# Kernel optimization log

Hardware: AMD Instinct MI355X
Metric: run time of the kernel (lower is better)

The kernel has to match this reference:

```python
import jax, jax.numpy as jnp
import numpy as np

TAU = 1.0      # gumbel-softmax temperature
ALPHA = 0.05   # mixprop alpha
GDEP = 1       # mixprop depth

B, C, H, W = 16, 512, 96, 96
N = 64  # n_classes / codebook size


def setup_inputs() -> dict:
    key = jax.random.key(0)
    ks = jax.random.split(key, 8)
    u = jax.random.uniform(ks[3], (B, N, H, W), dtype=jnp.float32, minval=1e-6, maxval=1.0 - 1e-6)
    gumbel_noise = -jnp.log(-jnp.log(u))  # standard Gumbel(0,1)
    return {
        "x": jax.random.normal(ks[0], (B, C, H, W), dtype=jnp.float32),
        "centers": jax.random.normal(ks[1], (N, C), dtype=jnp.float32) * 0.1,
        "A": jax.random.uniform(ks[2], (N, N), dtype=jnp.float32),
        "gumbel_noise": gumbel_noise,
        "W_bc": jax.random.normal(ks[4], (1, C), dtype=jnp.float32) * 0.05,
        "b_bc": jnp.zeros((1,), dtype=jnp.float32),
        "W_gcn": jax.random.normal(ks[5], (C, 2 * C), dtype=jnp.float32) * 0.03,
        "b_gcn": jnp.zeros((C,), dtype=jnp.float32),
    }


def _mixprop_centers(centers, A, W_gcn, b_gcn):
    # mixprop on the codebook: centers [N, C] viewed as x of shape [1, C, N, 1]
    n = A.shape[0]
    adj = A + jnp.eye(n, dtype=A.dtype)
    a = adj / adj.sum(axis=1, keepdims=True)           # row-normalized adjacency
    xg = centers.T[None, :, :, None]                    # [1, C, N, 1]
    h = xg
    outs = [h]
    for _ in range(GDEP):
        h = ALPHA * xg + (1.0 - ALPHA) * jnp.einsum('ncwl,vw->ncvl', h, a)
        outs.append(h)
    ho = jnp.concatenate(outs, axis=1)                  # [1, (GDEP+1)*C, N, 1]
    new_c = jnp.einsum('oc,bcvl->bovl', W_gcn, ho) + b_gcn[None, :, None, None]
    return new_c[0, :, :, 0].T                          # [N, C]


def reference(x, centers, A, gumbel_noise, W_bc, b_bc, W_gcn, b_gcn):
    n = centers.shape[0]
    # inner products of features with codebook centers
    inner_products = jnp.einsum('bchw,nc->bnhw', x, centers)          # [B, N, H, W]
    # gumbel-softmax with hard (straight-through) assignment over dim 1
    y = jax.nn.softmax((inner_products + gumbel_noise) / TAU, axis=1)
    hard = jax.nn.one_hot(jnp.argmax(y, axis=1), n, dtype=y.dtype, axis=1)
    one_hot = hard + y - jax.lax.stop_gradient(y)
    # quantized features via codebook gather
    z_q = jnp.einsum('bnhw,nd->bdhw', one_hot, centers)               # [B, C, H, W]
    # 1x1 conv binary classifier + global average pool
    heatmap = jnp.einsum('oc,bchw->bohw', W_bc, z_q) + b_bc[None, :, None, None]  # [B,1,H,W]
    logits = heatmap.mean(axis=(2, 3)).squeeze()                      # [B]
    # graph diffusion of the codebook
    new_centers = _mixprop_centers(centers, A, W_gcn, b_gcn)          # [N, C]
    normed_ip = jnp.einsum('bchw,nc->bnhw', x, new_centers)           # [B, N, H, W]
    cluster_probs = jax.nn.one_hot(jnp.argmax(normed_ip, axis=1), n, dtype=normed_ip.dtype, axis=1)
    cluster_loss = -(cluster_probs * jax.nn.softmax(normed_ip, axis=1)).sum(axis=1).mean()
    return heatmap, logits, cluster_loss, inner_products
```

## Files before the change

### kernel.cpp

```cpp
#include <hip/hip_runtime.h>
#include <math.h>

#define BATCH   16
#define CDIM    512
#define HWDIM   9216
#define NCLS    64
#define TILE    128
#define NTILES  72
#define NCHUNK  16

#define LOGOFF  147456
#define LOSSOFF 147472
#define IPOFF   147473

#define WS_CC   0
#define WS_S    65536
#define WS_PH   65600
#define WS_PC   66752
#define WS_AP   67904
#define WS_MIX  166208

typedef __attribute__((ext_vector_type(8))) short bf16x8;
typedef __attribute__((ext_vector_type(4))) float f32x4;

__device__ __forceinline__ void split3(float v, float& h, float& m, float& l) {
  float hf = __uint_as_float(__float_as_uint(v) & 0xFFFF0000u);
  float r  = v - hf;
  float mf = __uint_as_float(__float_as_uint(r) & 0xFFFF0000u);
  float r2 = r - mf;
  float lf = __uint_as_float(__float_as_uint(r2) & 0xFFFF0000u);
  h = hf; m = mf; l = lf;
}

__device__ __forceinline__ unsigned packbf(float a, float b) {
  return (__float_as_uint(a) >> 16) | (__float_as_uint(b) & 0xFFFF0000u);
}

__global__ __launch_bounds__(256) void prep1_kernel(
    const float* __restrict__ centers, const float* __restrict__ Aadj,
    const float* __restrict__ W_bc, const float* __restrict__ b_bc,
    float* __restrict__ ws) {
  __shared__ float a_n[NCLS];
  __shared__ float red[256];
  const int n = blockIdx.x;
  const int tid = threadIdx.x;

  if (tid < NCLS) a_n[tid] = Aadj[n * NCLS + tid] + (tid == n ? 1.0f : 0.0f);
  __syncthreads();
  if (tid == 0) {
    float ssum = 0.f;
    for (int w = 0; w < NCLS; ++w) ssum += a_n[w];
    red[0] = 1.0f / ssum;
  }
  __syncthreads();
  float inv = red[0];
  __syncthreads();
  if (tid < NCLS) a_n[tid] *= inv;
  __syncthreads();

  float p = 0.f;
  for (int c = tid; c < CDIM; c += 256) {
    float v = centers[n * CDIM + c];
    ws[WS_CC + n * CDIM + c] = v;
    float acc = 0.f;
    #pragma unroll 8
    for (int w = 0; w < NCLS; ++w) acc = fmaf(a_n[w], centers[w * CDIM + c], acc);
    ws[WS_MIX + n * CDIM + c] = 0.05f * v + 0.95f * acc;
    p = fmaf(W_bc[c], v, p);
  }
  red[tid] = p;
  __syncthreads();
  for (int st = 128; st > 0; st >>= 1) {
    if (tid < st) red[tid] += red[tid + st];
    __syncthreads();
  }
  if (tid == 0) ws[WS_S + n] = red[0] + b_bc[0];
}

__global__ __launch_bounds__(256) void prep2_kernel(
    const float* __restrict__ W_gcn, const float* __restrict__ b_gcn,
    float* __restrict__ ws) {
  __shared__ float catT[128][65];
  const int tid = threadIdx.x;
  const int oo = tid >> 6, n = tid & 63;
  const int o = blockIdx.x * 4 + oo;
  const float* Wrow = W_gcn + (size_t)o * 1024;
  float acc = b_gcn[o];

  for (int k0 = 0; k0 < 1024; k0 += 128) {
    __syncthreads();
    const float* srcb = (k0 < 512) ? (ws + WS_CC + k0) : (ws + WS_MIX + (k0 - 512));
    #pragma unroll
    for (int i = 0; i < 32; ++i) {
      int idx = i * 256 + tid;
      int kk = idx & 127, n2 = idx >> 7;
      catT[kk][n2] = srcb[(size_t)n2 * CDIM + kk];
    }
    __syncthreads();
    #pragma unroll 16
    for (int kk = 0; kk < 128; ++kk)
      acc = fmaf(Wrow[k0 + kk], catT[kk][n], acc);
  }
  ws[WS_CC + (size_t)(NCLS + n) * CDIM + o] = acc;
}

__global__ __launch_bounds__(256) void pack_kernel(float* __restrict__ ws) {
  const int gid = blockIdx.x * 256 + threadIdx.x;
  const int lane = gid & 63;
  const int mb = (gid >> 6) & 7;
  const int c = gid >> 9;
  const int row = mb * 16 + (lane & 15);
  const int kb = c * 32 + ((lane >> 4) & 3) * 8;
  const float* src = ws + WS_CC + (size_t)row * CDIM + kb;
  float e[8];
  *(float4*)&e[0] = *(const float4*)(src);
  *(float4*)&e[4] = *(const float4*)(src + 4);
  unsigned dh[4], dm[4], dl[4];
  #pragma unroll
  for (int d = 0; d < 4; ++d) {
    float h0, m0, l0, h1, m1, l1;
    split3(e[2 * d], h0, m0, l0);
    split3(e[2 * d + 1], h1, m1, l1);
    dh[d] = packbf(h0, h1); dm[d] = packbf(m0, m1); dl[d] = packbf(l0, l1);
  }
  const size_t base = WS_AP + (size_t)c * 6144 + (size_t)mb * 256 + (size_t)lane * 4;
  *(uint4*)(ws + base)        = make_uint4(dh[0], dh[1], dh[2], dh[3]);
  *(uint4*)(ws + base + 2048) = make_uint4(dm[0], dm[1], dm[2], dm[3]);
  *(uint4*)(ws + base + 4096) = make_uint4(dl[0], dl[1], dl[2], dl[3]);
}

__global__ __launch_bounds__(256, 3) void main_kernel(
    const float* __restrict__ x, const float* __restrict__ gumbel,
    float* __restrict__ ws, float* __restrict__ out) {
  __shared__ char ldsmem[49152];
  __shared__ float s_sh[NCLS];
  char* buf0 = ldsmem;
  char* buf1 = ldsmem + 24576;

  const int tid = threadIdx.x;
  const int w = tid >> 6, l = tid & 63;
  const int tile = blockIdx.x, b = blockIdx.y;
  const int hw0 = tile * TILE;

  if (tid < NCLS) s_sh[tid] = ws[WS_S + tid];

  const float* xb = x + (size_t)b * CDIM * HWDIM;
  const float* pB = xb + (size_t)(w * 8) * HWDIM + hw0 + l;
  const char* ap = (const char*)(ws + WS_AP);
  const int la16 = l * 16;

  f32x4 cip[8], cnp[8];
  #pragma unroll
  for (int i = 0; i < 8; ++i) {
    cip[i] = (f32x4){0.f, 0.f, 0.f, 0.f};
    cnp[i] = (f32x4){0.f, 0.f, 0.f, 0.f};
  }

  float bre[16];
  bf16x8 A0[5], A1[5];

#define LOAD_A(AS, c_) do {                                                   \
    const char* asrc = ap + (size_t)(c_) * 24576;                             \
    AS[0] = *(const bf16x8*)(asrc + w * 1024 + la16);                         \
    AS[1] = *(const bf16x8*)(asrc + 8192 + w * 1024 + la16);                  \
    AS[2] = *(const bf16x8*)(asrc + 16384 + w * 1024 + la16);                 \
    AS[3] = *(const bf16x8*)(asrc + (4 + w) * 1024 + la16);                   \
    AS[4] = *(const bf16x8*)(asrc + 8192 + (4 + w) * 1024 + la16);            \
  } while (0)

#define LOAD_B(c_) do {                                                       \
    const size_t koff = (size_t)(c_) * 32 * HWDIM;                            \
    _Pragma("unroll")                                                         \
    for (int j = 0; j < 8; ++j) {                                             \
      bre[j]     = pB[koff + (size_t)j * HWDIM];                              \
      bre[8 + j] = pB[koff + (size_t)j * HWDIM + 64];                         \
    }                                                                         \
  } while (0)

#define WRITE_B(WB) do {                                                      \
    _Pragma("unroll")                                                         \
    for (int hh = 0; hh < 2; ++hh) {                                          \
      unsigned dh[4], dm[4], dl[4];                                           \
      _Pragma("unroll")                                                       \
      for (int d = 0; d < 4; ++d) {                                           \
        float h0, m0, l0, h1, m1, l1;                                         \
        split3(bre[hh * 8 + 2 * d], h0, m0, l0);                              \
        split3(bre[hh * 8 + 2 * d + 1], h1, m1, l1);                          \
        dh[d] = packbf(h0, h1); dm[d] = packbf(m0, m1); dl[d] = packbf(l0, l1);\
      }                                                                       \
      char* basep = (WB) + ((((l >> 4) + hh * 4) * 64) + (w << 4) + (l & 15)) * 16; \
      *(uint4*)(basep)         = make_uint4(dh[0], dh[1], dh[2], dh[3]);      \
      *(uint4*)(basep + 8192)  = make_uint4(dm[0], dm[1], dm[2], dm[3]);      \
      *(uint4*)(basep + 16384) = make_uint4(dl[0], dl[1], dl[2], dl[3]);      \
    }                                                                         \
  } while (0)

#define LGKM_BARRIER() do {                                                   \
    asm volatile("s_waitcnt lgkmcnt(0)" ::: "memory");                        \
    __builtin_amdgcn_s_barrier();                                             \
    __builtin_amdgcn_sched_barrier(0);                                        \
  } while (0)

#define CHUNK(c_, RB, WB, AC, AN) do {                                        \
    if ((c_) + 1 < NCHUNK) { LOAD_A(AN, (c_) + 1); LOAD_B((c_) + 1); }        \
    _Pragma("unroll")                                                         \
    for (int nb = 0; nb < 8; ++nb) {                                          \
      bf16x8 bH = *(const bf16x8*)((RB) + nb * 1024 + la16);                  \
      bf16x8 bM = *(const bf16x8*)((RB) + 8192 + nb * 1024 + la16);           \
      bf16x8 bL = *(const bf16x8*)((RB) + 16384 + nb * 1024 + la16);          \
      cip[nb] = __builtin_amdgcn_mfma_f32_16x16x32_bf16(AC[0], bH, cip[nb], 0, 0, 0); \
      cip[nb] = __builtin_amdgcn_mfma_f32_16x16x32_bf16(AC[0], bM, cip[nb], 0, 0, 0); \
      cip[nb] = __builtin_amdgcn_mfma_f32_16x16x32_bf16(AC[1], bH, cip[nb], 0, 0, 0); \
      cip[nb] = __builtin_amdgcn_mfma_f32_16x16x32_bf16(AC[0], bL, cip[nb], 0, 0, 0); \
      cip[nb] = __builtin_amdgcn_mfma_f32_16x16x32_bf16(AC[1], bM, cip[nb], 0, 0, 0); \
      cip[nb] = __builtin_amdgcn_mfma_f32_16x16x32_bf16(AC[2], bH, cip[nb], 0, 0, 0); \
      cnp[nb] = __builtin_amdgcn_mfma_f32_16x16x32_bf16(AC[3], bH, cnp[nb], 0, 0, 0); \
      cnp[nb] = __builtin_amdgcn_mfma_f32_16x16x32_bf16(AC[3], bM, cnp[nb], 0, 0, 0); \
      cnp[nb] = __builtin_amdgcn_mfma_f32_16x16x32_bf16(AC[4], bH, cnp[nb], 0, 0, 0); \
    }                                                                         \
    if ((c_) + 1 < NCHUNK) WRITE_B(WB);                                       \
    LGKM_BARRIER();                                                           \
  } while (0)

  LOAD_A(A0, 0);
  LOAD_B(0);
  WRITE_B(buf0);
  LGKM_BARRIER();

  #pragma unroll 1
  for (int cc = 0; cc < NCHUNK; cc += 2) {
    CHUNK(cc, buf0, buf1, A0, A1);
    CHUNK(cc + 1, buf1, buf0, A1, A0);
  }

  float* pvv  = (float*)ldsmem;
  int*   pvi  = (int*)(ldsmem + 2048);
  float* pnm  = (float*)(ldsmem + 4096);
  float* pns  = (float*)(ldsmem + 6144);
  float* m2   = (float*)(ldsmem + 8192);
  float* hbuf = (float*)(ldsmem + 8704);
  float* cbuf = (float*)(ldsmem + 9216);

  const size_t bn = (size_t)b * NCLS;
  float* ipo = out + IPOFF;
  const int rbase = 16 * w + ((l >> 4) & 3) * 4;
  const int c15 = l & 15;

  float bv[8]; int bi[8]; float nm[8];
  #pragma unroll
  for (int nb = 0; nb < 8; ++nb) {
    const int hw = hw0 + nb * 16 + c15;
    float best = -1e30f; int besti = 0;
    #pragma unroll
    for (int r = 0; r < 4; ++r) {
      const int n = rbase + r;
      const float v = cip[nb][r];
      ipo[(bn + n) * HWDIM + hw] = v;
      const float t = v + gumbel[(bn + n) * HWDIM + hw];
      if (t > best) { best = t; besti = n; }
    }
    bv[nb] = best; bi[nb] = besti;
    float m = cnp[nb][0];
    m = fmaxf(m, cnp[nb][1]); m = fmaxf(m, cnp[nb][2]); m = fmaxf(m, cnp[nb][3]);
    nm[nb] = m;
  }
  #pragma unroll
  for (int nb = 0; nb < 8; ++nb) {
    #pragma unroll
    for (int mk = 16; mk <= 32; mk <<= 1) {
      float ov = __shfl_xor(bv[nb], mk);
      int   oi = __shfl_xor(bi[nb], mk);
      if (ov > bv[nb] || (ov == bv[nb] && oi < bi[nb])) { bv[nb] = ov; bi[nb] = oi; }
      nm[nb] = fmaxf(nm[nb], __shfl_xor(nm[nb], mk));
    }
  }
  __syncthreads();
  if ((l >> 4) == 0) {
    #pragma unroll
    for (int nb = 0; nb < 8; ++nb) {
      pvv[w * 128 + nb * 16 + l] = bv[nb];
      pvi[w * 128 + nb * 16 + l] = bi[nb];
      pnm[w * 128 + nb * 16 + l] = nm[nb];
    }
  }
  __syncthreads();

  if (tid < 128) {
    float v = pvv[tid]; int i = pvi[tid];
    #pragma unroll
    for (int ww = 1; ww < 4; ++ww) {
      float v2 = pvv[ww * 128 + tid]; int i2 = pvi[ww * 128 + tid];
      if (v2 > v || (v2 == v && i2 < i)) { v = v2; i = i2; }
    }
    float h = s_sh[i];
    hbuf[tid] = h;
    out[(size_t)b * HWDIM + hw0 + tid] = h;
    float m = pnm[tid];
    #pragma unroll
    for (int ww = 1; ww < 4; ++ww) m = fmaxf(m, pnm[ww * 128 + tid]);
    m2[tid] = m;
  }
  __syncthreads();

  #pragma unroll
  for (int nb = 0; nb < 8; ++nb) {
    const float mm = m2[nb * 16 + c15];
    float s = __expf(cnp[nb][0] - mm) + __expf(cnp[nb][1] - mm)
            + __expf(cnp[nb][2] - mm) + __expf(cnp[nb][3] - mm);
    s += __shfl_xor(s, 16);
    s += __shfl_xor(s, 32);
    if ((l >> 4) == 0) pns[w * 128 + nb * 16 + l] = s;
  }
  __syncthreads();

  if (tid < 128) {
    float S = pns[tid] + pns[128 + tid] + pns[256 + tid] + pns[384 + tid];
    cbuf[tid] = 1.0f / S;
  }
  __syncthreads();

  if (tid < 64) {
    float hs = hbuf[tid] + hbuf[tid + 64];
    float cs = cbuf[tid] + cbuf[tid + 64];
    #pragma unroll
    for (int o = 32; o > 0; o >>= 1) {
      hs += __shfl_down(hs, o);
      cs += __shfl_down(cs, o);
    }
    if (tid == 0) {
      ws[WS_PH + b * NTILES + tile] = hs;
      ws[WS_PC + b * NTILES + tile] = cs;
    }
  }
#undef LOAD_A
#undef LOAD_B
#undef WRITE_B
#undef CHUNK
#undef LGKM_BARRIER
}

__global__ __launch_bounds__(256) void finish_kernel(
    const float* __restrict__ ws, float* __restrict__ out) {
  __shared__ double sred[256];
  const int tid = threadIdx.x;
  {
    int bb = tid >> 4, lane = tid & 15;
    double s = 0.0;
    for (int t = lane; t < NTILES; t += 16) s += (double)ws[WS_PH + bb * NTILES + t];
    #pragma unroll
    for (int o = 8; o > 0; o >>= 1) s += __shfl_down(s, o, 16);
    if (lane == 0) out[LOGOFF + bb] = (float)(s / (double)HWDIM);
  }
  double c = 0.0;
  for (int i = tid; i < BATCH * NTILES; i += 256) c += (double)ws[WS_PC + i];
  sred[tid] = c;
  __syncthreads();
  for (int st = 128; st > 0; st >>= 1) {
    if (tid < st) sred[tid] += sred[tid + st];
    __syncthreads();
  }
  if (tid == 0) out[LOSSOFF] = (float)(-sred[0] / (double)(BATCH * HWDIM));
}

extern "C" void kernel_launch(void* const* d_in, const int* in_sizes, int n_in,
                              void* d_out, int out_size, void* d_ws, size_t ws_size,
                              hipStream_t stream) {
  const float* x       = (const float*)d_in[0];
  const float* centers = (const float*)d_in[1];
  const float* Aadj    = (const float*)d_in[2];
  const float* gumbel  = (const float*)d_in[3];
  const float* W_bc    = (const float*)d_in[4];
  const float* b_bc    = (const float*)d_in[5];
  const float* W_gcn   = (const float*)d_in[6];
  const float* b_gcn   = (const float*)d_in[7];
  float* out = (float*)d_out;
  float* ws  = (float*)d_ws;

  hipLaunchKernelGGL(prep1_kernel, dim3(NCLS), dim3(256), 0, stream,
                     centers, Aadj, W_bc, b_bc, ws);
  hipLaunchKernelGGL(prep2_kernel, dim3(128), dim3(256), 0, stream,
                     W_gcn, b_gcn, ws);
  hipLaunchKernelGGL(pack_kernel, dim3(32), dim3(256), 0, stream, ws);
  hipLaunchKernelGGL(main_kernel, dim3(NTILES, BATCH), dim3(256), 0, stream,
                     x, gumbel, ws, out);
  hipLaunchKernelGGL(finish_kernel, dim3(1), dim3(256), 0, stream, ws, out);
}
```

Baseline: 207.0 us.

## Halve spatial tile to 64 columns, raise occupancy, add MFMA priority hints

Shrinks the per-block HW tile from 128 to 64 columns, doubling the grid, halving LDS and accumulator registers, and raising the launch-bounds occupancy target from 3 to 4 blocks. It also raises wave priority around the MFMA phase, adds a scheduling barrier after the prefetch loads, and moves the partial-sum workspace slots so they overlap the codebook region. The aim is more waves in flight to hide global-load latency. The cost is that each B-chunk load and split now feeds half as many MFMAs, so A-fragment loads and barriers per FLOP double.

New measurement: 224.3 us. +8.4%, slower.

```diff
diff --git a/kernel.cpp b/kernel.cpp
--- a/kernel.cpp
+++ b/kernel.cpp
@@ -5,8 +5,8 @@
 #define CDIM    512
 #define HWDIM   9216
 #define NCLS    64
-#define TILE    128
-#define NTILES  72
+#define TILE    64
+#define NTILES  144
 #define NCHUNK  16
 
 #define LOGOFF  147456
@@ -14,9 +14,9 @@
 #define IPOFF   147473
 
 #define WS_CC   0
+#define WS_PH   0
+#define WS_PC   2304
 #define WS_S    65536
-#define WS_PH   65600
-#define WS_PC   66752
 #define WS_AP   67904
 #define WS_MIX  166208
 
@@ -129,16 +129,17 @@
   *(uint4*)(ws + base + 4096) = make_uint4(dl[0], dl[1], dl[2], dl[3]);
 }
 
-__global__ __launch_bounds__(256, 3) void main_kernel(
+__global__ __launch_bounds__(256, 4) void main_kernel(
     const float* __restrict__ x, const float* __restrict__ gumbel,
     float* __restrict__ ws, float* __restrict__ out) {
-  __shared__ char ldsmem[49152];
+  __shared__ char ldsmem[24576];
   __shared__ float s_sh[NCLS];
   char* buf0 = ldsmem;
-  char* buf1 = ldsmem + 24576;
+  char* buf1 = ldsmem + 12288;
 
   const int tid = threadIdx.x;
   const int w = tid >> 6, l = tid & 63;
+  const int q = l >> 4, c15 = l & 15;
   const int tile = blockIdx.x, b = blockIdx.y;
   const int hw0 = tile * TILE;
 
@@ -149,14 +150,14 @@
   const char* ap = (const char*)(ws + WS_AP);
   const int la16 = l * 16;
 
-  f32x4 cip[8], cnp[8];
+  f32x4 cip[4], cnp[4];
   #pragma unroll
-  for (int i = 0; i < 8; ++i) {
+  for (int i = 0; i < 4; ++i) {
     cip[i] = (f32x4){0.f, 0.f, 0.f, 0.f};
     cnp[i] = (f32x4){0.f, 0.f, 0.f, 0.f};
   }
 
-  float bre[16];
+  float bre[8];
   bf16x8 A0[5], A1[5];
 
 #define LOAD_A(AS, c_) do {                                                   \
@@ -171,28 +172,22 @@
 #define LOAD_B(c_) do {                                                       \
     const size_t koff = (size_t)(c_) * 32 * HWDIM;                            \
     _Pragma("unroll")                                                         \
-    for (int j = 0; j < 8; ++j) {                                             \
-      bre[j]     = pB[koff + (size_t)j * HWDIM];                              \
-      bre[8 + j] = pB[koff + (size_t)j * HWDIM + 64];                         \
+    for (int j = 0; j < 8; ++j) bre[j] = pB[koff + (size_t)j * HWDIM];        \
+  } while (0)
+
+#define WRITE_B(WB) do {                                                      \
+    unsigned dh[4], dm[4], dl[4];                                             \
+    _Pragma("unroll")                                                         \
+    for (int d = 0; d < 4; ++d) {                                             \
+      float h0, m0, l0, h1, m1, l1;                                           \
+      split3(bre[2 * d], h0, m0, l0);                                         \
+      split3(bre[2 * d + 1], h1, m1, l1);                                     \
+      dh[d] = packbf(h0, h1); dm[d] = packbf(m0, m1); dl[d] = packbf(l0, l1); \
     }                                                                         \
-  } while (0)
-
-#define WRITE_B(WB) do {                                                      \
-    _Pragma("unroll")                                                         \
-    for (int hh = 0; hh < 2; ++hh) {                                          \
-      unsigned dh[4], dm[4], dl[4];                                           \
-      _Pragma("unroll")                                                       \
-      for (int d = 0; d < 4; ++d) {                                           \
-        float h0, m0, l0, h1, m1, l1;                                         \
-        split3(bre[hh * 8 + 2 * d], h0, m0, l0);                              \
-        split3(bre[hh * 8 + 2 * d + 1], h1, m1, l1);                          \
-        dh[d] = packbf(h0, h1); dm[d] = packbf(m0, m1); dl[d] = packbf(l0, l1);\
-      }                                                                       \
-      char* basep = (WB) + ((((l >> 4) + hh * 4) * 64) + (w << 4) + (l & 15)) * 16; \
-      *(uint4*)(basep)         = make_uint4(dh[0], dh[1], dh[2], dh[3]);      \
-      *(uint4*)(basep + 8192)  = make_uint4(dm[0], dm[1], dm[2], dm[3]);      \
-      *(uint4*)(basep + 16384) = make_uint4(dl[0], dl[1], dl[2], dl[3]);      \
-    }                                                                         \
+    char* basep = (WB) + (q * 1024 + w * 256 + c15 * 16);                     \
+    *(uint4*)(basep)        = make_uint4(dh[0], dh[1], dh[2], dh[3]);         \
+    *(uint4*)(basep + 4096) = make_uint4(dm[0], dm[1], dm[2], dm[3]);         \
+    *(uint4*)(basep + 8192) = make_uint4(dl[0], dl[1], dl[2], dl[3]);         \
   } while (0)
 
 #define LGKM_BARRIER() do {                                                   \
@@ -201,13 +196,13 @@
     __builtin_amdgcn_sched_barrier(0);                                        \
   } while (0)
 
-#define CHUNK(c_, RB, WB, AC, AN) do {                                        \
-    if ((c_) + 1 < NCHUNK) { LOAD_A(AN, (c_) + 1); LOAD_B((c_) + 1); }        \
+#define PHASE(RB, AC) do {                                                    \
+    __builtin_amdgcn_s_setprio(1);                                            \
     _Pragma("unroll")                                                         \
-    for (int nb = 0; nb < 8; ++nb) {                                          \
+    for (int nb = 0; nb < 4; ++nb) {                                          \
       bf16x8 bH = *(const bf16x8*)((RB) + nb * 1024 + la16);                  \
-      bf16x8 bM = *(const bf16x8*)((RB) + 8192 + nb * 1024 + la16);           \
-      bf16x8 bL = *(const bf16x8*)((RB) + 16384 + nb * 1024 + la16);          \
+      bf16x8 bM = *(const bf16x8*)((RB) + 4096 + nb * 1024 + la16);           \
+      bf16x8 bL = *(const bf16x8*)((RB) + 8192 + nb * 1024 + la16);           \
       cip[nb] = __builtin_amdgcn_mfma_f32_16x16x32_bf16(AC[0], bH, cip[nb], 0, 0, 0); \
       cip[nb] = __builtin_amdgcn_mfma_f32_16x16x32_bf16(AC[0], bM, cip[nb], 0, 0, 0); \
       cip[nb] = __builtin_amdgcn_mfma_f32_16x16x32_bf16(AC[1], bH, cip[nb], 0, 0, 0); \
@@ -218,6 +213,16 @@
       cnp[nb] = __builtin_amdgcn_mfma_f32_16x16x32_bf16(AC[3], bM, cnp[nb], 0, 0, 0); \
       cnp[nb] = __builtin_amdgcn_mfma_f32_16x16x32_bf16(AC[4], bH, cnp[nb], 0, 0, 0); \
     }                                                                         \
+    __builtin_amdgcn_s_setprio(0);                                            \
+  } while (0)
+
+#define CHUNK(c_, RB, WB, AC, AN) do {                                        \
+    if ((c_) + 1 < NCHUNK) {                                                  \
+      LOAD_A(AN, (c_) + 1);                                                   \
+      LOAD_B((c_) + 1);                                                       \
+      __builtin_amdgcn_sched_barrier(0);                                      \
+    }                                                                         \
+    PHASE(RB, AC);                                                            \
     if ((c_) + 1 < NCHUNK) WRITE_B(WB);                                       \
     LGKM_BARRIER();                                                           \
   } while (0)
@@ -234,62 +239,54 @@
   }
 
   float* pvv  = (float*)ldsmem;
-  int*   pvi  = (int*)(ldsmem + 2048);
-  float* pnm  = (float*)(ldsmem + 4096);
-  float* pns  = (float*)(ldsmem + 6144);
-  float* m2   = (float*)(ldsmem + 8192);
-  float* hbuf = (float*)(ldsmem + 8704);
-  float* cbuf = (float*)(ldsmem + 9216);
+  int*   pvi  = (int*)(ldsmem + 1024);
+  float* pnm  = (float*)(ldsmem + 2048);
+  float* pns  = (float*)(ldsmem + 3072);
+  float* m2   = (float*)(ldsmem + 4096);
+  float* hbuf = (float*)(ldsmem + 4352);
+  float* cbuf = (float*)(ldsmem + 4608);
 
   const size_t bn = (size_t)b * NCLS;
   float* ipo = out + IPOFF;
-  const int rbase = 16 * w + ((l >> 4) & 3) * 4;
-  const int c15 = l & 15;
-
-  float bv[8]; int bi[8]; float nm[8];
+
   #pragma unroll
-  for (int nb = 0; nb < 8; ++nb) {
-    const int hw = hw0 + nb * 16 + c15;
-    float best = -1e30f; int besti = 0;
+  for (int nb = 0; nb < 4; ++nb) {
+    const int col = nb * 16 + c15;
+    const int gcol = hw0 + col;
+    float best = -1e30f; int bi = 0;
     #pragma unroll
     for (int r = 0; r < 4; ++r) {
-      const int n = rbase + r;
+      const int n = 16 * w + q * 4 + r;
+      const size_t off = (bn + n) * HWDIM + gcol;
       const float v = cip[nb][r];
-      ipo[(bn + n) * HWDIM + hw] = v;
-      const float t = v + gumbel[(bn + n) * HWDIM + hw];
-      if (t > best) { best = t; besti = n; }
-    }
-    bv[nb] = best; bi[nb] = besti;
-    float m = cnp[nb][0];
-    m = fmaxf(m, cnp[nb][1]); m = fmaxf(m, cnp[nb][2]); m = fmaxf(m, cnp[nb][3]);
-    nm[nb] = m;
-  }
-  #pragma unroll
-  for (int nb = 0; nb < 8; ++nb) {
+      ipo[off] = v;
+      const float t = v + gumbel[off];
+      if (t > best) { best = t; bi = n; }
+    }
     #pragma unroll
     for (int mk = 16; mk <= 32; mk <<= 1) {
-      float ov = __shfl_xor(bv[nb], mk);
-      int   oi = __shfl_xor(bi[nb], mk);
-      if (ov > bv[nb] || (ov == bv[nb] && oi < bi[nb])) { bv[nb] = ov; bi[nb] = oi; }
-      nm[nb] = fmaxf(nm[nb], __shfl_xor(nm[nb], mk));
-    }
-  }
-  __syncthreads();
-  if ((l >> 4) == 0) {
-    #pragma unroll
-    for (int nb = 0; nb < 8; ++nb) {
-      pvv[w * 128 + nb * 16 + l] = bv[nb];
-      pvi[w * 128 + nb * 16 + l] = bi[nb];
-      pnm[w * 128 + nb * 16 + l] = nm[nb];
-    }
-  }
-  __syncthreads();
-
-  if (tid < 128) {
+      float ov = __shfl_xor(best, mk);
+      int   oi = __shfl_xor(bi, mk);
+      if (ov > best || (ov == best && oi < bi)) { best = ov; bi = oi; }
+    }
+    float mx = -1e30f;
+    #pragma unroll
+    for (int r = 0; r < 4; ++r) mx = fmaxf(mx, cnp[nb][r]);
+    #pragma unroll
+    for (int mk = 16; mk <= 32; mk <<= 1) mx = fmaxf(mx, __shfl_xor(mx, mk));
+    if (q == 0) {
+      pvv[w * 64 + col] = best;
+      pvi[w * 64 + col] = bi;
+      pnm[w * 64 + col] = mx;
+    }
+  }
+  __syncthreads();
+
+  if (tid < 64) {
     float v = pvv[tid]; int i = pvi[tid];
     #pragma unroll
     for (int ww = 1; ww < 4; ++ww) {
-      float v2 = pvv[ww * 128 + tid]; int i2 = pvi[ww * 128 + tid];
+      float v2 = pvv[ww * 64 + tid]; int i2 = pvi[ww * 64 + tid];
       if (v2 > v || (v2 == v && i2 < i)) { v = v2; i = i2; }
     }
     float h = s_sh[i];
@@ -297,31 +294,32 @@
     out[(size_t)b * HWDIM + hw0 + tid] = h;
     float m = pnm[tid];
     #pragma unroll
-    for (int ww = 1; ww < 4; ++ww) m = fmaxf(m, pnm[ww * 128 + tid]);
+    for (int ww = 1; ww < 4; ++ww) m = fmaxf(m, pnm[ww * 64 + tid]);
     m2[tid] = m;
   }
   __syncthreads();
 
   #pragma unroll
-  for (int nb = 0; nb < 8; ++nb) {
-    const float mm = m2[nb * 16 + c15];
+  for (int nb = 0; nb < 4; ++nb) {
+    const int col = nb * 16 + c15;
+    const float mm = m2[col];
     float s = __expf(cnp[nb][0] - mm) + __expf(cnp[nb][1] - mm)
             + __expf(cnp[nb][2] - mm) + __expf(cnp[nb][3] - mm);
     s += __shfl_xor(s, 16);
     s += __shfl_xor(s, 32);
-    if ((l >> 4) == 0) pns[w * 128 + nb * 16 + l] = s;
-  }
-  __syncthreads();
-
-  if (tid < 128) {
-    float S = pns[tid] + pns[128 + tid] + pns[256 + tid] + pns[384 + tid];
+    if (q == 0) pns[w * 64 + col] = s;
+  }
+  __syncthreads();
+
+  if (tid < 64) {
+    float S = pns[tid] + pns[64 + tid] + pns[128 + tid] + pns[192 + tid];
     cbuf[tid] = 1.0f / S;
   }
   __syncthreads();
 
   if (tid < 64) {
-    float hs = hbuf[tid] + hbuf[tid + 64];
-    float cs = cbuf[tid] + cbuf[tid + 64];
+    float hs = hbuf[tid];
+    float cs = cbuf[tid];
     #pragma unroll
     for (int o = 32; o > 0; o >>= 1) {
       hs += __shfl_down(hs, o);
@@ -335,6 +333,7 @@
 #undef LOAD_A
 #undef LOAD_B
 #undef WRITE_B
+#undef PHASE
 #undef CHUNK
 #undef LGKM_BARRIER
 }
```
